# Kernel optimization log

Measured on AMD Instinct MI355X. Metric: run time of the kernel, lower is better.

The kernel has to match this reference:

```python
import jax, jax.numpy as jnp
import numpy as np

N, D, H, L, E = 50000, 128, 3, 2, 500000  # nodes, feat dim, hops, mp layers, edges/hop


def setup_inputs() -> dict:
    key = jax.random.key(0)
    ks = jax.random.split(key, 5)
    x = jax.random.normal(ks[0], (N, D), dtype=jnp.float32)
    # 2-layer bias-free MLP per (layer, hop); scaled for stable magnitudes
    w1 = jax.random.normal(ks[1], (L, H, D, D), dtype=jnp.float32) / np.sqrt(D).astype(np.float32)
    w2 = jax.random.normal(ks[2], (L, H, D, D), dtype=jnp.float32) / np.sqrt(D).astype(np.float32)
    eps = jnp.full((1,), 0.1, dtype=jnp.float32)  # nn.Parameter(ones(1)*0.1)
    scatter_idx = jax.random.randint(ks[3], (H, E), 0, N)  # gather source nodes per hop
    node_idx = jax.random.randint(ks[4], (H, E), 0, N)     # scatter destination nodes per hop
    return {"x": x, "w1": w1, "w2": w2, "eps": eps,
            "scatter_idx": scatter_idx, "node_idx": node_idx}


def reference(x, w1, w2, eps, scatter_idx, node_idx):
    # LocalWL message passing: per layer, out = (1+eps)*x + sum_hops MLP_hop(x + scatter_sum(x[src], dst))
    for l in range(L):
        out = (1.0 + eps) * x
        for hop in range(H):
            h_v = x[scatter_idx[hop]]                                   # [E, D] gather
            agg = jax.ops.segment_sum(h_v, node_idx[hop], num_segments=N)
            h = x + agg                                                  # scatter_reduce 'sum', include_self=True
            h = jax.nn.relu(h @ w1[l, hop]) @ w2[l, hop]                 # 2-layer MLP, no bias, no final act
            out = out + h                                                # hop_pool='sum'; dropout p=0 (eval)
        x = out
    return x
```

## Files before the change

### kernel.cpp

```cpp
#include <hip/hip_runtime.h>

#define NN 50000
#define DD 128
#define HH 3
#define LL 2
#define EE 500000
#define NT 782
#define NT64 (NT * 64)
#define WE 36
#define CAP 1024
#define CHUNK 8192
#define NCH ((EE + CHUNK - 1) / CHUNK)
#define NSTRIP32 ((NN + 31) / 32)

using short8v  = __attribute__((ext_vector_type(8))) short;
using f32x4    = __attribute__((ext_vector_type(4))) float;

__device__ __forceinline__ ushort f2bf_rne(float x) {
    union { float f; uint u; } c; c.f = x;
    uint u = c.u;
    uint r = (u + 0x7FFFu + ((u >> 16) & 1u)) >> 16;
    return (ushort)r;
}
__device__ __forceinline__ float blo(uint v) { union { uint u; float f; } c; c.u = v << 16; return c.f; }
__device__ __forceinline__ float bhi(uint v) { union { uint u; float f; } c; c.u = v & 0xFFFF0000u; return c.f; }
__device__ __forceinline__ uint packbf(float a, float b) {
    return (uint)f2bf_rne(a) | ((uint)f2bf_rne(b) << 16);
}
__device__ __forceinline__ int pkpos(int gi) { return (gi & 3) * 2 + (gi >> 2); }
__device__ __forceinline__ int pk_us(int k)  { return (k & ~31) + pkpos((k & 31) >> 2) * 4 + (k & 3); }
__device__ __forceinline__ int pk_pair(int q) { return (q & ~15) + pkpos((q & 15) >> 1) * 2 + (q & 1); }

__global__ void prep_x_kernel(const float* __restrict__ x, uint* __restrict__ xbf) {
    int i = blockIdx.x * blockDim.x + threadIdx.x;
    if (i >= NN * 64) return;
    int row = i >> 6, q = i & 63;
    float2 v = ((const float2*)x)[i];
    xbf[(size_t)row * 64 + pk_pair(q)] = packbf(v.x, v.y);
}

__global__ void prep_w_kernel(const float* __restrict__ w1, const float* __restrict__ w2,
                              ushort* __restrict__ wbf) {
    int t = blockIdx.x * blockDim.x + threadIdx.x;
    if (t >= 12 * 16384) return;
    int mi = t >> 14;
    int r  = t & 16383;
    int nn = r >> 7;
    int kk = r & 127;
    const float* W = (mi < 6) ? (w1 + (size_t)mi * 16384) : (w2 + (size_t)(mi - 6) * 16384);
    int ct  = nn >> 4, l15 = nn & 15;
    int ks  = kk >> 5, rr  = kk & 31;
    int lg  = (rr & 15) >> 2;
    int j   = (rr & 3) + (rr >> 4) * 4;
    wbf[(size_t)mi * 16384 + (((ct * 4 + ks) * 4 + lg) * 16 + l15) * 8 + j] =
        f2bf_rne(W[kk * 128 + nn]);
}

__global__ void cursor_init_kernel(int* __restrict__ cursor) {
    int i = blockIdx.x * blockDim.x + threadIdx.x;
    if (i < HH * NT) cursor[i] = i * CAP;
}

__global__ __launch_bounds__(256)
void fill_staged_kernel(const int* __restrict__ src, const int* __restrict__ dst,
                        int* __restrict__ cursor, uint* __restrict__ bins) {
    __shared__ int  cnt[NT];
    __shared__ int  ofs[NT];
    __shared__ int  gbase[NT];
    __shared__ int  part[256];
    __shared__ uint stage[CHUNK];
    const int hop  = blockIdx.y;
    const int base = blockIdx.x * CHUNK;
    const int tid  = threadIdx.x;
    const int end  = min(base + CHUNK, EE);
    const int* d = dst + (size_t)hop * EE;
    const int* s = src + (size_t)hop * EE;

    for (int i = tid; i < NT; i += 256) cnt[i] = 0;
    __syncthreads();
    for (int i = base + tid; i < end; i += 256) atomicAdd(&cnt[d[i] >> 6], 1);
    __syncthreads();

    int l[4];
    const int b0 = tid * 4;
    #pragma unroll
    for (int j = 0; j < 4; ++j) {
        int b = b0 + j;
        l[j] = (b < NT) ? cnt[b] : 0;
    }
    part[tid] = l[0] + l[1] + l[2] + l[3];
    __syncthreads();
    for (int off = 1; off < 256; off <<= 1) {
        int v = (tid >= off) ? part[tid - off] : 0;
        __syncthreads();
        part[tid] += v;
        __syncthreads();
    }
    int e = (tid == 0) ? 0 : part[tid - 1];
    #pragma unroll
    for (int j = 0; j < 4; ++j) {
        int b = b0 + j;
        if (b < NT) { ofs[b] = e; e += l[j]; }
    }
    __syncthreads();
    for (int i = tid; i < NT; i += 256) cnt[i] = ofs[i];
    __syncthreads();

    for (int i = base + tid; i < end; i += 256) {
        int dd = d[i];
        int t2 = dd >> 6;
        int slot = atomicAdd(&cnt[t2], 1);
        stage[slot] = ((uint)t2 << 22) | ((uint)s[i] << 6) | (uint)(dd & 63);
    }
    __syncthreads();

    for (int b = tid; b < NT; b += 256) {
        int len = cnt[b] - ofs[b];
        gbase[b] = len ? atomicAdd(&cursor[hop * NT + b], len) : 0;
    }
    __syncthreads();

    const int total = end - base;
    for (int i = tid; i < total; i += 256) {
        uint v = stage[i];
        int b = (int)(v >> 22);
        bins[gbase[b] + (i - ofs[b])] = v & 0x3FFFFFu;
    }
}

__global__ __launch_bounds__(256)
void ell_build_kernel(const uint* __restrict__ bins, const int* __restrict__ cursor,
                      uint* __restrict__ ell, int* __restrict__ counts) {
    __shared__ int  scnt[64];
    __shared__ uint sell[64 * WE];
    const int tile = blockIdx.x;
    const int hop  = blockIdx.y;
    const int tid  = threadIdx.x;
    if (tid < 64) scnt[tid] = 0;
    __syncthreads();
    const int b0 = (hop * NT + tile) * CAP;
    const int b1 = cursor[hop * NT + tile];
    for (int j = b0 + tid; j < b1; j += 256) {
        uint pk = bins[j];
        int dlo = (int)(pk & 63u);
        int slot = atomicAdd(&scnt[dlo], 1);
        if (slot < WE) sell[dlo * WE + slot] = pk >> 6;
    }
    __syncthreads();
    if (tid < 64) {
        int c = scnt[tid];
        counts[(size_t)hop * NT64 + tile * 64 + tid] = (c > WE) ? WE : c;
    }
    uint4* dstp = (uint4*)(ell + ((size_t)hop * NT + tile) * 64 * WE);
    const uint4* srcp = (const uint4*)sell;
    for (int i = tid; i < 64 * WE / 4; i += 256) dstp[i] = srcp[i];
}

__global__ __launch_bounds__(256)
void gather_kernel(const uint* __restrict__ xbf, const int* __restrict__ counts,
                   const uint* __restrict__ ell, uint* __restrict__ hbuf) {
    const int node = blockIdx.x * 4 + (threadIdx.x >> 6);
    const uint lane = threadIdx.x & 63;
    if (node >= NN) return;
    const uint sv = xbf[(uint)node * 64u + lane];
    const float sx = blo(sv), sy = bhi(sv);
    #pragma unroll
    for (int hop = 0; hop < HH; ++hop) {
        int c = counts[hop * NT64 + node];
        if (c > WE) c = WE;
        const uint* el = ell + (uint)(hop * NT64 + node) * WE;
        float ax = sx, ay = sy;
        float bx = 0.f, by = 0.f, cx = 0.f, cy = 0.f, dx = 0.f, dy = 0.f;
        int i = 0;
        for (; i + 8 <= c; i += 8) {
            uint4 s4a = *(const uint4*)(el + i);
            uint4 s4b = *(const uint4*)(el + i + 4);
            uint v0 = xbf[s4a.x * 64u + lane];
            uint v1 = xbf[s4a.y * 64u + lane];
            uint v2 = xbf[s4a.z * 64u + lane];
            uint v3 = xbf[s4a.w * 64u + lane];
            uint v4 = xbf[s4b.x * 64u + lane];
            uint v5 = xbf[s4b.y * 64u + lane];
            uint v6 = xbf[s4b.z * 64u + lane];
            uint v7 = xbf[s4b.w * 64u + lane];
            ax += blo(v0); ay += bhi(v0);
            bx += blo(v1); by += bhi(v1);
            cx += blo(v2); cy += bhi(v2);
            dx += blo(v3); dy += bhi(v3);
            ax += blo(v4); ay += bhi(v4);
            bx += blo(v5); by += bhi(v5);
            cx += blo(v6); cy += bhi(v6);
            dx += blo(v7); dy += bhi(v7);
        }
        for (; i + 4 <= c; i += 4) {
            uint4 s4 = *(const uint4*)(el + i);
            uint v0 = xbf[s4.x * 64u + lane];
            uint v1 = xbf[s4.y * 64u + lane];
            uint v2 = xbf[s4.z * 64u + lane];
            uint v3 = xbf[s4.w * 64u + lane];
            ax += blo(v0); ay += bhi(v0);
            bx += blo(v1); by += bhi(v1);
            cx += blo(v2); cy += bhi(v2);
            dx += blo(v3); dy += bhi(v3);
        }
        for (; i < c; ++i) {
            uint v = xbf[el[i] * 64u + lane];
            ax += blo(v); ay += bhi(v);
        }
        ax += bx + cx + dx;
        ay += by + cy + dy;
        hbuf[(uint)(hop * NN + node) * 64u + lane] = packbf(ax, ay);
    }
}

__global__ __launch_bounds__(256)
void mlp3_kernel(const uint* __restrict__ hbuf, const uint* __restrict__ xbf_in,
                 const ushort* __restrict__ wbf, const float* __restrict__ eps,
                 float* __restrict__ outf, uint* __restrict__ outbf, int layer) {
    __shared__ __align__(16) ushort sBuf[2 * 32 * 128];
    ushort* hS = sBuf;
    ushort* tS = sBuf + 32 * 128;

    const int tid = threadIdx.x;
    const int l   = tid & 63;
    const int w   = tid >> 6;
    const int row0 = blockIdx.x * 32;
    const int l15 = l & 15;
    const int lg  = l >> 4;
    const int sr  = tid >> 4;
    const int scc = tid & 15;

    f32x4 accO[2][2];
    #pragma unroll
    for (int rt = 0; rt < 2; ++rt)
        #pragma unroll
        for (int j = 0; j < 2; ++j) accO[rt][j] = (f32x4){0.f,0.f,0.f,0.f};

    const int g0 = min(row0 + sr, NN - 1);
    const int g1 = min(row0 + sr + 16, NN - 1);
    const int c0 = scc ^ (sr & 7);
    const int c1 = scc ^ ((sr + 16) & 7);
    {
        uint4 st0 = *(const uint4*)(hbuf + ((size_t)0 * NN + g0) * 64 + c0 * 4);
        uint4 st1 = *(const uint4*)(hbuf + ((size_t)0 * NN + g1) * 64 + c1 * 4);
        *(uint4*)(hS + sr * 128 + scc * 8)        = st0;
        *(uint4*)(hS + (sr + 16) * 128 + scc * 8) = st1;
    }
    uint4 pf0 = *(const uint4*)(hbuf + ((size_t)1 * NN + g0) * 64 + c0 * 4);
    uint4 pf1 = *(const uint4*)(hbuf + ((size_t)1 * NN + g1) * 64 + c1 * 4);
    __syncthreads();

    #pragma unroll
    for (int hop = 0; hop < HH; ++hop) {
        const ushort* W1p = wbf + (size_t)(layer * HH + hop) * 16384;
        const ushort* W2p = wbf + (size_t)(6 + layer * HH + hop) * 16384;

        f32x4 acc[2][2];
        #pragma unroll
        for (int rt = 0; rt < 2; ++rt)
            #pragma unroll
            for (int j = 0; j < 2; ++j) acc[rt][j] = (f32x4){0.f,0.f,0.f,0.f};
        #pragma unroll
        for (int ks = 0; ks < 4; ++ks) {
            const int ch = (ks * 4 + lg) ^ (l15 & 7);
            short8v A0 = *(const short8v*)(hS + l15 * 128 + ch * 8);
            short8v A1 = *(const short8v*)(hS + (16 + l15) * 128 + ch * 8);
            short8v B0 = *(const short8v*)(W1p + (((w * 2 + 0) * 4 + ks) * 64 + l) * 8);
            short8v B1 = *(const short8v*)(W1p + (((w * 2 + 1) * 4 + ks) * 64 + l) * 8);
            acc[0][0] = __builtin_amdgcn_mfma_f32_16x16x32_bf16(A0, B0, acc[0][0], 0, 0, 0);
            acc[0][1] = __builtin_amdgcn_mfma_f32_16x16x32_bf16(A0, B1, acc[0][1], 0, 0, 0);
            acc[1][0] = __builtin_amdgcn_mfma_f32_16x16x32_bf16(A1, B0, acc[1][0], 0, 0, 0);
            acc[1][1] = __builtin_amdgcn_mfma_f32_16x16x32_bf16(A1, B1, acc[1][1], 0, 0, 0);
        }
        #pragma unroll
        for (int rt = 0; rt < 2; ++rt) {
            #pragma unroll
            for (int j = 0; j < 2; ++j) {
                const int us = pk_us((w * 2 + j) * 16 + l15);
                #pragma unroll
                for (int r = 0; r < 4; ++r) {
                    const int row = rt * 16 + lg * 4 + r;
                    const int ch  = (us >> 3) ^ (row & 7);
                    tS[row * 128 + ch * 8 + (us & 7)] = f2bf_rne(fmaxf(acc[rt][j][r], 0.f));
                }
            }
        }
        __syncthreads();

        if (hop + 1 < HH) {
            *(uint4*)(hS + sr * 128 + scc * 8)        = pf0;
            *(uint4*)(hS + (sr + 16) * 128 + scc * 8) = pf1;
            if (hop + 2 < HH) {
                pf0 = *(const uint4*)(hbuf + ((size_t)(hop + 2) * NN + g0) * 64 + c0 * 4);
                pf1 = *(const uint4*)(hbuf + ((size_t)(hop + 2) * NN + g1) * 64 + c1 * 4);
            }
        }

        #pragma unroll
        for (int ks = 0; ks < 4; ++ks) {
            const int ch = (ks * 4 + lg) ^ (l15 & 7);
            short8v A0 = *(const short8v*)(tS + l15 * 128 + ch * 8);
            short8v A1 = *(const short8v*)(tS + (16 + l15) * 128 + ch * 8);
            short8v B0 = *(const short8v*)(W2p + (((w * 2 + 0) * 4 + ks) * 64 + l) * 8);
            short8v B1 = *(const short8v*)(W2p + (((w * 2 + 1) * 4 + ks) * 64 + l) * 8);
            accO[0][0] = __builtin_amdgcn_mfma_f32_16x16x32_bf16(A0, B0, accO[0][0], 0, 0, 0);
            accO[0][1] = __builtin_amdgcn_mfma_f32_16x16x32_bf16(A0, B1, accO[0][1], 0, 0, 0);
            accO[1][0] = __builtin_amdgcn_mfma_f32_16x16x32_bf16(A1, B0, accO[1][0], 0, 0, 0);
            accO[1][1] = __builtin_amdgcn_mfma_f32_16x16x32_bf16(A1, B1, accO[1][1], 0, 0, 0);
        }
        __syncthreads();
    }

    float* fw = (float*)sBuf;
    #pragma unroll
    for (int rt = 0; rt < 2; ++rt) {
        #pragma unroll
        for (int j = 0; j < 2; ++j) {
            const int col = (w * 2 + j) * 16 + l15;
            #pragma unroll
            for (int r = 0; r < 4; ++r) {
                const int row = rt * 16 + lg * 4 + r;
                const int ch  = (col >> 2) ^ (row & 7);
                fw[row * 128 + ch * 4 + (col & 3)] = accO[rt][j][r];
            }
        }
    }
    __syncthreads();

    const float s = 1.0f + eps[0];
    #pragma unroll
    for (int it = 0; it < 4; ++it) {
        const int cid = tid + it * 256;
        const int row = cid >> 5;
        const int c4  = cid & 31;
        const int ch  = c4 ^ (row & 7);
        const int gr  = row0 + row;
        if (gr < NN) {
            f32x4 a = *(const f32x4*)(fw + row * 128 + ch * 4);
            const int q0 = pk_pair(2 * c4), q1 = pk_pair(2 * c4 + 1);
            const uint xv0 = xbf_in[(size_t)gr * 64 + q0];
            const uint xv1 = xbf_in[(size_t)gr * 64 + q1];
            a[0] += s * blo(xv0);
            a[1] += s * bhi(xv0);
            a[2] += s * blo(xv1);
            a[3] += s * bhi(xv1);
            if (outf != nullptr) {
                *(f32x4*)(outf + (size_t)gr * DD + c4 * 4) = a;
            } else {
                outbf[(size_t)gr * 64 + q0] = packbf(a[0], a[1]);
                outbf[(size_t)gr * 64 + q1] = packbf(a[2], a[3]);
            }
        }
    }
}

extern "C" void kernel_launch(void* const* d_in, const int* in_sizes, int n_in,
                              void* d_out, int out_size, void* d_ws, size_t ws_size,
                              hipStream_t stream) {
    const float* x    = (const float*)d_in[0];
    const float* w1   = (const float*)d_in[1];
    const float* w2   = (const float*)d_in[2];
    const float* eps  = (const float*)d_in[3];
    const int*   sidx = (const int*)d_in[4];
    const int*   nidx = (const int*)d_in[5];
    float* out = (float*)d_out;

    uint*   xbf    = (uint*)d_ws;
    uint*   hbuf   = xbf + (size_t)NN * 64;
    uint*   bins   = hbuf;
    ushort* wbf    = (ushort*)(hbuf + (size_t)HH * NN * 64);
    uint*   ell    = (uint*)(wbf + 12 * 16384);
    int*    counts = (int*)(ell + (size_t)HH * NT64 * WE);
    int*    cursor = counts + HH * NT64;

    cursor_init_kernel<<<(HH * NT + 255) / 256, 256, 0, stream>>>(cursor);
    prep_x_kernel<<<(NN * 64 + 255) / 256, 256, 0, stream>>>(x, xbf);
    prep_w_kernel<<<(12 * 16384 + 255) / 256, 256, 0, stream>>>(w1, w2, wbf);

    dim3 sgrid(NCH, HH);
    fill_staged_kernel<<<sgrid, 256, 0, stream>>>(sidx, nidx, cursor, bins);
    dim3 bgrid(NT, HH);
    ell_build_kernel<<<bgrid, 256, 0, stream>>>(bins, cursor, ell, counts);

    const int ggrid = (NN + 3) / 4;

    gather_kernel<<<ggrid, 256, 0, stream>>>(xbf, counts, ell, hbuf);
    mlp3_kernel<<<NSTRIP32, 256, 0, stream>>>(hbuf, xbf, wbf, eps, nullptr, xbf, 0);
    gather_kernel<<<ggrid, 256, 0, stream>>>(xbf, counts, ell, hbuf);
    mlp3_kernel<<<NSTRIP32, 256, 0, stream>>>(hbuf, xbf, wbf, eps, out, nullptr, 1);
}
```

Before: 229.2 us.

## Fuse neighbor gather into per-strip MLP kernel with double-buffered hops

```diff
diff --git a/kernel.cpp b/kernel.cpp
--- a/kernel.cpp
+++ b/kernel.cpp
@@ -157,78 +157,21 @@
 }
 
 __global__ __launch_bounds__(256)
-void gather_kernel(const uint* __restrict__ xbf, const int* __restrict__ counts,
-                   const uint* __restrict__ ell, uint* __restrict__ hbuf) {
-    const int node = blockIdx.x * 4 + (threadIdx.x >> 6);
-    const uint lane = threadIdx.x & 63;
-    if (node >= NN) return;
-    const uint sv = xbf[(uint)node * 64u + lane];
-    const float sx = blo(sv), sy = bhi(sv);
-    #pragma unroll
-    for (int hop = 0; hop < HH; ++hop) {
-        int c = counts[hop * NT64 + node];
-        if (c > WE) c = WE;
-        const uint* el = ell + (uint)(hop * NT64 + node) * WE;
-        float ax = sx, ay = sy;
-        float bx = 0.f, by = 0.f, cx = 0.f, cy = 0.f, dx = 0.f, dy = 0.f;
-        int i = 0;
-        for (; i + 8 <= c; i += 8) {
-            uint4 s4a = *(const uint4*)(el + i);
-            uint4 s4b = *(const uint4*)(el + i + 4);
-            uint v0 = xbf[s4a.x * 64u + lane];
-            uint v1 = xbf[s4a.y * 64u + lane];
-            uint v2 = xbf[s4a.z * 64u + lane];
-            uint v3 = xbf[s4a.w * 64u + lane];
-            uint v4 = xbf[s4b.x * 64u + lane];
-            uint v5 = xbf[s4b.y * 64u + lane];
-            uint v6 = xbf[s4b.z * 64u + lane];
-            uint v7 = xbf[s4b.w * 64u + lane];
-            ax += blo(v0); ay += bhi(v0);
-            bx += blo(v1); by += bhi(v1);
-            cx += blo(v2); cy += bhi(v2);
-            dx += blo(v3); dy += bhi(v3);
-            ax += blo(v4); ay += bhi(v4);
-            bx += blo(v5); by += bhi(v5);
-            cx += blo(v6); cy += bhi(v6);
-            dx += blo(v7); dy += bhi(v7);
-        }
-        for (; i + 4 <= c; i += 4) {
-            uint4 s4 = *(const uint4*)(el + i);
-            uint v0 = xbf[s4.x * 64u + lane];
-            uint v1 = xbf[s4.y * 64u + lane];
-            uint v2 = xbf[s4.z * 64u + lane];
-            uint v3 = xbf[s4.w * 64u + lane];
-            ax += blo(v0); ay += bhi(v0);
-            bx += blo(v1); by += bhi(v1);
-            cx += blo(v2); cy += bhi(v2);
-            dx += blo(v3); dy += bhi(v3);
-        }
-        for (; i < c; ++i) {
-            uint v = xbf[el[i] * 64u + lane];
-            ax += blo(v); ay += bhi(v);
-        }
-        ax += bx + cx + dx;
-        ay += by + cy + dy;
-        hbuf[(uint)(hop * NN + node) * 64u + lane] = packbf(ax, ay);
-    }
-}
-
-__global__ __launch_bounds__(256)
-void mlp3_kernel(const uint* __restrict__ hbuf, const uint* __restrict__ xbf_in,
-                 const ushort* __restrict__ wbf, const float* __restrict__ eps,
-                 float* __restrict__ outf, uint* __restrict__ outbf, int layer) {
-    __shared__ __align__(16) ushort sBuf[2 * 32 * 128];
-    ushort* hS = sBuf;
-    ushort* tS = sBuf + 32 * 128;
+void fused3_kernel(const uint* __restrict__ xbf, const int* __restrict__ counts,
+                   const uint* __restrict__ ell, const ushort* __restrict__ wbf,
+                   const float* __restrict__ eps,
+                   float* __restrict__ outf, uint* __restrict__ outbf, int layer) {
+    __shared__ __align__(16) ushort sBuf[3 * 32 * 128];
+    ushort* hA = sBuf;
+    ushort* hB = sBuf + 4096;
+    ushort* tS = sBuf + 8192;
 
     const int tid = threadIdx.x;
-    const int l   = tid & 63;
+    const uint lane = tid & 63;
     const int w   = tid >> 6;
     const int row0 = blockIdx.x * 32;
-    const int l15 = l & 15;
-    const int lg  = l >> 4;
-    const int sr  = tid >> 4;
-    const int scc = tid & 15;
+    const int l15 = tid & 15;
+    const int lg  = ((int)lane) >> 4;
 
     f32x4 accO[2][2];
     #pragma unroll
@@ -236,24 +179,54 @@
         #pragma unroll
         for (int j = 0; j < 2; ++j) accO[rt][j] = (f32x4){0.f,0.f,0.f,0.f};
 
-    const int g0 = min(row0 + sr, NN - 1);
-    const int g1 = min(row0 + sr + 16, NN - 1);
-    const int c0 = scc ^ (sr & 7);
-    const int c1 = scc ^ ((sr + 16) & 7);
-    {
-        uint4 st0 = *(const uint4*)(hbuf + ((size_t)0 * NN + g0) * 64 + c0 * 4);
-        uint4 st1 = *(const uint4*)(hbuf + ((size_t)0 * NN + g1) * 64 + c1 * 4);
-        *(uint4*)(hS + sr * 128 + scc * 8)        = st0;
-        *(uint4*)(hS + (sr + 16) * 128 + scc * 8) = st1;
-    }
-    uint4 pf0 = *(const uint4*)(hbuf + ((size_t)1 * NN + g0) * 64 + c0 * 4);
-    uint4 pf1 = *(const uint4*)(hbuf + ((size_t)1 * NN + g1) * 64 + c1 * 4);
+    auto gather_rows = [&](ushort* dstS, int gh) {
+        uint* du = (uint*)dstS;
+        #pragma unroll 2
+        for (int rr8 = 0; rr8 < 8; ++rr8) {
+            const int rl = w * 8 + rr8;
+            const int node = row0 + rl;
+            float ax = 0.f, ay = 0.f, bx = 0.f, by = 0.f;
+            float cx = 0.f, cy = 0.f, dx = 0.f, dy = 0.f;
+            if (node < NN) {
+                const uint sv = xbf[(uint)node * 64u + lane];
+                ax = blo(sv); ay = bhi(sv);
+                int c = counts[gh * NT64 + node];
+                if (c > WE) c = WE;
+                const uint* el = ell + (uint)(gh * NT64 + node) * WE;
+                int i = 0;
+                for (; i + 4 <= c; i += 4) {
+                    uint4 s4 = *(const uint4*)(el + i);
+                    uint v0 = xbf[s4.x * 64u + lane];
+                    uint v1 = xbf[s4.y * 64u + lane];
+                    uint v2 = xbf[s4.z * 64u + lane];
+                    uint v3 = xbf[s4.w * 64u + lane];
+                    ax += blo(v0); ay += bhi(v0);
+                    bx += blo(v1); by += bhi(v1);
+                    cx += blo(v2); cy += bhi(v2);
+                    dx += blo(v3); dy += bhi(v3);
+                }
+                for (; i < c; ++i) {
+                    uint v = xbf[el[i] * 64u + lane];
+                    ax += blo(v); ay += bhi(v);
+                }
+                ax += bx + cx + dx;
+                ay += by + cy + dy;
+            }
+            du[rl * 64 + (((lane >> 2) ^ (uint)(rl & 7)) << 2) + (lane & 3)] = packbf(ax, ay);
+        }
+    };
+
+    gather_rows(hA, 0);
     __syncthreads();
 
     #pragma unroll
     for (int hop = 0; hop < HH; ++hop) {
         const ushort* W1p = wbf + (size_t)(layer * HH + hop) * 16384;
         const ushort* W2p = wbf + (size_t)(6 + layer * HH + hop) * 16384;
+        ushort* hS = (hop & 1) ? hB : hA;
+        ushort* nS = (hop & 1) ? hA : hB;
+
+        if (hop + 1 < HH) gather_rows(nS, hop + 1);
 
         f32x4 acc[2][2];
         #pragma unroll
@@ -265,8 +238,8 @@
             const int ch = (ks * 4 + lg) ^ (l15 & 7);
             short8v A0 = *(const short8v*)(hS + l15 * 128 + ch * 8);
             short8v A1 = *(const short8v*)(hS + (16 + l15) * 128 + ch * 8);
-            short8v B0 = *(const short8v*)(W1p + (((w * 2 + 0) * 4 + ks) * 64 + l) * 8);
-            short8v B1 = *(const short8v*)(W1p + (((w * 2 + 1) * 4 + ks) * 64 + l) * 8);
+            short8v B0 = *(const short8v*)(W1p + (((w * 2 + 0) * 4 + ks) * 64 + (int)lane) * 8);
+            short8v B1 = *(const short8v*)(W1p + (((w * 2 + 1) * 4 + ks) * 64 + (int)lane) * 8);
             acc[0][0] = __builtin_amdgcn_mfma_f32_16x16x32_bf16(A0, B0, acc[0][0], 0, 0, 0);
             acc[0][1] = __builtin_amdgcn_mfma_f32_16x16x32_bf16(A0, B1, acc[0][1], 0, 0, 0);
             acc[1][0] = __builtin_amdgcn_mfma_f32_16x16x32_bf16(A1, B0, acc[1][0], 0, 0, 0);
@@ -287,22 +260,13 @@
         }
         __syncthreads();
 
-        if (hop + 1 < HH) {
-            *(uint4*)(hS + sr * 128 + scc * 8)        = pf0;
-            *(uint4*)(hS + (sr + 16) * 128 + scc * 8) = pf1;
-            if (hop + 2 < HH) {
-                pf0 = *(const uint4*)(hbuf + ((size_t)(hop + 2) * NN + g0) * 64 + c0 * 4);
-                pf1 = *(const uint4*)(hbuf + ((size_t)(hop + 2) * NN + g1) * 64 + c1 * 4);
-            }
-        }
-
         #pragma unroll
         for (int ks = 0; ks < 4; ++ks) {
             const int ch = (ks * 4 + lg) ^ (l15 & 7);
             short8v A0 = *(const short8v*)(tS + l15 * 128 + ch * 8);
             short8v A1 = *(const short8v*)(tS + (16 + l15) * 128 + ch * 8);
-            short8v B0 = *(const short8v*)(W2p + (((w * 2 + 0) * 4 + ks) * 64 + l) * 8);
-            short8v B1 = *(const short8v*)(W2p + (((w * 2 + 1) * 4 + ks) * 64 + l) * 8);
+            short8v B0 = *(const short8v*)(W2p + (((w * 2 + 0) * 4 + ks) * 64 + (int)lane) * 8);
+            short8v B1 = *(const short8v*)(W2p + (((w * 2 + 1) * 4 + ks) * 64 + (int)lane) * 8);
             accO[0][0] = __builtin_amdgcn_mfma_f32_16x16x32_bf16(A0, B0, accO[0][0], 0, 0, 0);
             accO[0][1] = __builtin_amdgcn_mfma_f32_16x16x32_bf16(A0, B1, accO[0][1], 0, 0, 0);
             accO[1][0] = __builtin_amdgcn_mfma_f32_16x16x32_bf16(A1, B0, accO[1][0], 0, 0, 0);
@@ -338,8 +302,8 @@
         if (gr < NN) {
             f32x4 a = *(const f32x4*)(fw + row * 128 + ch * 4);
             const int q0 = pk_pair(2 * c4), q1 = pk_pair(2 * c4 + 1);
-            const uint xv0 = xbf_in[(size_t)gr * 64 + q0];
-            const uint xv1 = xbf_in[(size_t)gr * 64 + q1];
+            const uint xv0 = xbf[(size_t)gr * 64 + q0];
+            const uint xv1 = xbf[(size_t)gr * 64 + q1];
             a[0] += s * blo(xv0);
             a[1] += s * bhi(xv0);
             a[2] += s * blo(xv1);
@@ -366,12 +330,12 @@
     float* out = (float*)d_out;
 
     uint*   xbf    = (uint*)d_ws;
-    uint*   hbuf   = xbf + (size_t)NN * 64;
-    uint*   bins   = hbuf;
-    ushort* wbf    = (ushort*)(hbuf + (size_t)HH * NN * 64);
+    uint*   xbf2   = xbf + (size_t)NN * 64;
+    ushort* wbf    = (ushort*)(xbf2 + (size_t)NN * 64);
     uint*   ell    = (uint*)(wbf + 12 * 16384);
     int*    counts = (int*)(ell + (size_t)HH * NT64 * WE);
     int*    cursor = counts + HH * NT64;
+    uint*   bins   = (uint*)(cursor + HH * NT);
 
     cursor_init_kernel<<<(HH * NT + 255) / 256, 256, 0, stream>>>(cursor);
     prep_x_kernel<<<(NN * 64 + 255) / 256, 256, 0, stream>>>(x, xbf);
@@ -382,10 +346,6 @@
     dim3 bgrid(NT, HH);
     ell_build_kernel<<<bgrid, 256, 0, stream>>>(bins, cursor, ell, counts);
 
-    const int ggrid = (NN + 3) / 4;
-
-    gather_kernel<<<ggrid, 256, 0, stream>>>(xbf, counts, ell, hbuf);
-    mlp3_kernel<<<NSTRIP32, 256, 0, stream>>>(hbuf, xbf, wbf, eps, nullptr, xbf, 0);
-    gather_kernel<<<ggrid, 256, 0, stream>>>(xbf, counts, ell, hbuf);
-    mlp3_kernel<<<NSTRIP32, 256, 0, stream>>>(hbuf, xbf, wbf, eps, out, nullptr, 1);
-}
+    fused3_kernel<<<NSTRIP32, 256, 0, stream>>>(xbf,  counts, ell, wbf, eps, nullptr, xbf2, 0);
+    fused3_kernel<<<NSTRIP32, 256, 0, stream>>>(xbf2, counts, ell, wbf, eps, out,  nullptr, 1);
+}
```

New measurement: 367.0 us. +60.1%, slower.
